# Performance work log

Hardware: AMD Instinct MI355X
Metric: run time of the kernel (lower is better)

## Reference

```python
import jax, jax.numpy as jnp
import numpy as np

QLEN, B, D = 1024, 4, 512
H, DH = 8, 64
MEM, DMLP = 1024, 2048
KLEN = MEM + QLEN
EPS = 1e-5


def layer_norm(x, g, b):
    mu = jnp.mean(x, axis=-1, keepdims=True)
    var = jnp.var(x, axis=-1, keepdims=True)
    return (x - mu) * jax.lax.rsqrt(var + EPS) * g + b


def rel_shift(x):
    # x: [qlen, klen, b, h] -- Transformer-XL relative shift trick
    q, k, b, h = x.shape
    zp = jnp.zeros((q, 1, b, h), dtype=x.dtype)
    x = jnp.concatenate([zp, x], axis=1)          # [q, k+1, b, h]
    x = x.reshape(k + 1, q, b, h)[1:]             # drop first row
    return x.reshape(q, k, b, h)


def setup_inputs() -> dict:
    key = jax.random.key(0)
    ks = jax.random.split(key, 12)
    s = 0.02
    inp = {
        "inputs": jax.random.normal(ks[0], (QLEN, B, D), jnp.float32),
        "r": jax.random.normal(ks[1], (KLEN, D), jnp.float32),
        "u": jax.random.normal(ks[2], (H, DH), jnp.float32) * s,
        "v": jax.random.normal(ks[3], (H, DH), jnp.float32) * s,
        "mem": jax.random.normal(ks[4], (MEM, B, D), jnp.float32),
        # causal mask: query i (global pos MEM+i) cannot attend key j > MEM+i
        "attn_mask": jnp.arange(KLEN)[None, :] > (jnp.arange(QLEN)[:, None] + MEM),
        "Wqkv": jax.random.normal(ks[5], (3 * D, D), jnp.float32) * s,
        "Wr": jax.random.normal(ks[6], (D, D), jnp.float32) * s,
        "Wo": jax.random.normal(ks[7], (D, D), jnp.float32) * s,
        "ln1_g": jnp.ones((D,), jnp.float32),
        "ln1_b": jnp.zeros((D,), jnp.float32),
        "mlp_w1": jax.random.normal(ks[8], (DMLP, D), jnp.float32) * s,
        "mlp_b1": jnp.zeros((DMLP,), jnp.float32),
        "mlp_w2": jax.random.normal(ks[9], (D, DMLP), jnp.float32) * s,
        "mlp_b2": jnp.zeros((D,), jnp.float32),
        "ln2_g": jnp.ones((D,), jnp.float32),
        "ln2_b": jnp.zeros((D,), jnp.float32),
    }
    return inp


def reference(inputs, r, u, v, mem, attn_mask, Wqkv, Wr, Wo,
              ln1_g, ln1_b, mlp_w1, mlp_b1, mlp_w2, mlp_b2, ln2_g, ln2_b):
    qlen, b, d = inputs.shape
    cat = jnp.concatenate([mem, inputs], axis=0)          # [klen, b, d]
    klen = cat.shape[0]
    qkv = cat @ Wqkv.T                                    # [klen, b, 3d]
    q, k, w_v = jnp.split(qkv, 3, axis=-1)
    q = q[-qlen:].reshape(qlen, b, H, DH)
    k = k.reshape(klen, b, H, DH)
    w_v = w_v.reshape(klen, b, H, DH)
    rk = (r @ Wr.T).reshape(klen, H, DH)                  # [klen, h, dh]

    AC = jnp.einsum('ibhd,jbhd->ijbh', q + u, k)          # content term
    BD = jnp.einsum('ibhd,jhd->ijbh', q + v, rk)          # position term
    BD = rel_shift(BD)
    scale = 1.0 / np.sqrt(DH)
    score = (AC + BD) * scale                             # [q, k, b, h]
    score = jnp.where(attn_mask[:, :, None, None], jnp.float32(-1e30), score)
    prob = jax.nn.softmax(score, axis=1)
    attn = jnp.einsum('ijbh,jbhd->ibhd', prob, w_v).reshape(qlen, b, d)
    attn_out = attn @ Wo.T

    y = layer_norm(inputs + attn_out, ln1_g, ln1_b)
    h = jax.nn.relu(y @ mlp_w1.T + mlp_b1)
    z = h @ mlp_w2.T + mlp_b2
    out = layer_norm(y + z, ln2_g, ln2_b)
    return out, prob
```

## Files before the change

### kernel.cpp

```cpp
#include <hip/hip_runtime.h>
#include <math.h>

#define QL 1024
#define BSZ 4
#define DM 512
#define NH 8
#define DHH 64
#define MEML 1024
#define KL 2048
#define DMLP 2048

typedef __attribute__((ext_vector_type(8))) short bf16x8;
typedef __attribute__((ext_vector_type(4))) float f32x4;

#define MFMA16(A, B, C) __builtin_amdgcn_mfma_f32_16x16x32_bf16((A), (B), (C), 0, 0, 0)
#define SWZB(r, cb) (((r) << 7) + ((cb) ^ (((r) & 7) << 4)))
#define RINGB(r, c) (((r) << 9) + ((((c) << 2)) ^ (((r) & 7) << 4)))
#define CVT2(dst, lo, hi) \
  asm("v_cvt_pk_bf16_f32 %0, %1, %2" : "=v"(dst) : "v"(lo), "v"(hi))
#define GLOAD_LDS(gp, lp) __builtin_amdgcn_global_load_lds( \
    (const __attribute__((address_space(1))) void*)(gp), \
    (__attribute__((address_space(3))) void*)(lp), 16, 0, 0)

__device__ __forceinline__ void split_bf16(const float4 a, uint2& h, uint2& l) {
  CVT2(h.x, a.x, a.y); CVT2(h.y, a.z, a.w);
  float4 r;
  r.x = a.x - __uint_as_float(h.x << 16);
  r.y = a.y - __uint_as_float(h.x & 0xffff0000u);
  r.z = a.z - __uint_as_float(h.y << 16);
  r.w = a.w - __uint_as_float(h.y & 0xffff0000u);
  CVT2(l.x, r.x, r.y); CVT2(l.y, r.z, r.w);
}

__device__ __forceinline__ void store_tiled(char* hiB, char* loB, int KT,
                                            int row, int c0, uint2 h, uint2 l) {
  const size_t off = (((size_t)(row >> 7) * KT + (c0 >> 6)) << 14)
                   + SWZB(row & 127, (c0 & 63) * 2);
  *(uint2*)(hiB + off) = h;
  *(uint2*)(loB + off) = l;
}

__global__ __launch_bounds__(256)
void precvt_early(const float* __restrict__ mem, const float* __restrict__ inputs,
                  const float* __restrict__ r, const float* __restrict__ Wqkv,
                  const float* __restrict__ Wr,
                  unsigned short* CAThi, unsigned short* CATlo,
                  unsigned short* Rhi, unsigned short* Rlo,
                  unsigned short* Qhi, unsigned short* Qlo,
                  unsigned short* WrHi, unsigned short* WrLo) {
  const int id = blockIdx.x * 256 + threadIdx.x;
  float4 a; uint2 h, l;
  if (id < 1048576) {
    const int row = id >> 7, c0 = (id & 127) * 4;
    const float* s = (row < 4096) ? mem + (size_t)row * 512
                                  : inputs + (size_t)(row - 4096) * 512;
    a = *(const float4*)(s + c0);
    split_bf16(a, h, l);
    store_tiled((char*)CAThi, (char*)CATlo, 8, row, c0, h, l);
  } else if (id < 1310720) {
    const int e = id - 1048576, row = e >> 7, c0 = (e & 127) * 4;
    a = *(const float4*)(r + (size_t)row * 512 + c0);
    split_bf16(a, h, l);
    store_tiled((char*)Rhi, (char*)Rlo, 8, row, c0, h, l);
  } else if (id < 1507328) {
    const int e = id - 1310720, row = e >> 7, c0 = (e & 127) * 4;
    a = *(const float4*)(Wqkv + (size_t)row * 512 + c0);
    split_bf16(a, h, l);
    store_tiled((char*)Qhi, (char*)Qlo, 8, row, c0, h, l);
  } else if (id < 1572864) {
    const int e = id - 1507328, row = e >> 7, c0 = (e & 127) * 4;
    a = *(const float4*)(Wr + (size_t)row * 512 + c0);
    split_bf16(a, h, l);
    store_tiled((char*)WrHi, (char*)WrLo, 8, row, c0, h, l);
  }
}

__global__ __launch_bounds__(256)
void precvt_late(const float* __restrict__ Wo, const float* __restrict__ w1,
                 const float* __restrict__ w2,
                 unsigned short* WoHi, unsigned short* WoLo,
                 unsigned short* w1Hi, unsigned short* w1Lo,
                 unsigned short* w2Hi, unsigned short* w2Lo) {
  const int id = blockIdx.x * 256 + threadIdx.x;
  float4 a; uint2 h, l;
  if (id < 65536) {
    const int row = id >> 7, c0 = (id & 127) * 4;
    a = *(const float4*)(Wo + (size_t)row * 512 + c0);
    split_bf16(a, h, l);
    store_tiled((char*)WoHi, (char*)WoLo, 8, row, c0, h, l);
  } else if (id < 327680) {
    const int e = id - 65536, row = e >> 7, c0 = (e & 127) * 4;
    a = *(const float4*)(w1 + (size_t)row * 512 + c0);
    split_bf16(a, h, l);
    store_tiled((char*)w1Hi, (char*)w1Lo, 8, row, c0, h, l);
  } else if (id < 589824) {
    const int e = id - 327680, row = e >> 9, c0 = (e & 511) * 4;
    a = *(const float4*)(w2 + (size_t)row * 2048 + c0);
    split_bf16(a, h, l);
    store_tiled((char*)w2Hi, (char*)w2Lo, 32, row, c0, h, l);
  }
}

template<int BM, bool AGLDS, bool BIAS, bool RELU>
__global__ __launch_bounds__(256)
void gemm_nt_mfma(const float* __restrict__ A0, const float* __restrict__ A1, int M0,
                  const unsigned short* __restrict__ AhiT, const unsigned short* __restrict__ AloT,
                  const unsigned short* __restrict__ WhiT, const unsigned short* __restrict__ WloT,
                  const float* __restrict__ bias,
                  float* __restrict__ C, int M, int N, int K) {
  constexpr int MR = 4;
  constexpr int NR = (BM == 128) ? 4 : 2;
  constexpr int AU = BM / 16;
  __shared__ __align__(16) unsigned short Ahi[BM * 64];
  __shared__ __align__(16) unsigned short Alo[BM * 64];
  __shared__ __align__(16) unsigned short Bhi[128 * 64];
  __shared__ __align__(16) unsigned short Blo[128 * 64];

  const int t = threadIdx.x;
  const int w = t >> 6, lane = t & 63;
  const int lq = lane & 15, lg = lane >> 4;
  const int row0 = blockIdx.y * BM, col0 = blockIdx.x * 128;
  const int wrow0 = (BM == 128) ? (w >> 1) * 64 : 0;
  const int wcol0 = (BM == 128) ? (w & 1) * 64 : w * 32;
  const int KT = K >> 6;
  const size_t amt = (size_t)(row0 >> 7) * KT;
  const int asub = (row0 & 127) << 7;
  const size_t bnt = (size_t)(col0 >> 7) * KT;

  float4 paf[AU];
  auto loadA = [&](int k0) {
    if (!AGLDS) {
      #pragma unroll
      for (int it = 0; it < AU; ++it) {
        const int idx = it * 256 + t;
        const int row = idx >> 4, c4 = (idx & 15) * 4;
        const int grow = row0 + row;
        const float* src = (grow < M0) ? (A0 + (size_t)grow * K)
                                       : (A1 + (size_t)(grow - M0) * K);
        paf[it] = *(const float4*)(src + k0 + c4);
      }
    }
  };

  f32x4 acc[MR][NR];
  #pragma unroll
  for (int m = 0; m < MR; ++m)
    #pragma unroll
    for (int n = 0; n < NR; ++n)
      acc[m][n] = (f32x4){0.f, 0.f, 0.f, 0.f};

  loadA(0);
  for (int kt = 0; kt < KT; ++kt) {
    __syncthreads();
    {
      const char* gbh = (const char*)WhiT + ((bnt + kt) << 14);
      const char* gbl = (const char*)WloT + ((bnt + kt) << 14);
      #pragma unroll
      for (int i = 0; i < 4; ++i) {
        const int off = (w * 4 + i) * 1024;
        GLOAD_LDS(gbh + off + lane * 16, (char*)Bhi + off);
        GLOAD_LDS(gbl + off + lane * 16, (char*)Blo + off);
      }
    }
    if (AGLDS) {
      const char* gah = (const char*)AhiT + ((amt + kt) << 14) + asub;
      const char* gal = (const char*)AloT + ((amt + kt) << 14) + asub;
      #pragma unroll
      for (int i = 0; i < BM / 32; ++i) {
        const int off = (w * (BM / 32) + i) * 1024;
        GLOAD_LDS(gah + off + lane * 16, (char*)Ahi + off);
        GLOAD_LDS(gal + off + lane * 16, (char*)Alo + off);
      }
    } else {
      #pragma unroll
      for (int it = 0; it < AU; ++it) {
        const int idx = it * 256 + t;
        const int row = idx >> 4, cb = (idx & 15) * 8;
        uint2 hi, lo;
        split_bf16(paf[it], hi, lo);
        *(uint2*)((char*)Ahi + SWZB(row, cb)) = hi;
        *(uint2*)((char*)Alo + SWZB(row, cb)) = lo;
      }
    }
    __syncthreads();
    if (!AGLDS && kt + 1 < KT) loadA((kt + 1) * 64);
    #pragma unroll
    for (int ks = 0; ks < 2; ++ks) {
      bf16x8 ah[MR], al[MR], bh[NR], bl[NR];
      #pragma unroll
      for (int m = 0; m < MR; ++m) {
        ah[m] = *(const bf16x8*)((const char*)Ahi + SWZB(wrow0 + m * 16 + lq, ks * 64 + lg * 16));
        al[m] = *(const bf16x8*)((const char*)Alo + SWZB(wrow0 + m * 16 + lq, ks * 64 + lg * 16));
      }
      #pragma unroll
      for (int n = 0; n < NR; ++n) {
        bh[n] = *(const bf16x8*)((const char*)Bhi + SWZB(wcol0 + n * 16 + lq, ks * 64 + lg * 16));
        bl[n] = *(const bf16x8*)((const char*)Blo + SWZB(wcol0 + n * 16 + lq, ks * 64 + lg * 16));
      }
      #pragma unroll
      for (int m = 0; m < MR; ++m)
        #pragma unroll
        for (int n = 0; n < NR; ++n) {
          acc[m][n] = MFMA16(ah[m], bh[n], acc[m][n]);
          acc[m][n] = MFMA16(ah[m], bl[n], acc[m][n]);
          acc[m][n] = MFMA16(al[m], bh[n], acc[m][n]);
        }
    }
  }
  #pragma unroll
  for (int n = 0; n < NR; ++n) {
    const int col = col0 + wcol0 + n * 16 + lq;
    const float bv = BIAS ? bias[col] : 0.f;
    #pragma unroll
    for (int m = 0; m < MR; ++m) {
      #pragma unroll
      for (int rg = 0; rg < 4; ++rg) {
        const int row = row0 + wrow0 + m * 16 + lg * 4 + rg;
        float vv = acc[m][n][rg] + bv;
        if (RELU) vv = fmaxf(vv, 0.f);
        C[(size_t)row * N + col] = vv;
      }
    }
  }
}

__global__ __launch_bounds__(256)
void attn2_kernel(const float* __restrict__ QKV, const float* __restrict__ RK,
                  const float* __restrict__ u, const float* __restrict__ v,
                  unsigned short* __restrict__ P, float* __restrict__ INV,
                  float* __restrict__ ATTN) {
  const int b = blockIdx.y;
  const int h = blockIdx.z;
  const int i0 = (((h >> 2) & 1) ? (15 - (int)blockIdx.x) : (int)blockIdx.x) * 64;
  const int t = threadIdx.x;
  const int w = t >> 6;
  const int lane = t & 63;
  const int lq = lane & 15;
  const int lg = lane >> 4;

  __shared__ __align__(16) unsigned short Ks[4096];
  __shared__ __align__(16) unsigned short Rs[4096];
  __shared__ __align__(16) unsigned short Vt[4096];
  __shared__ __align__(16) unsigned short Es[4096];
  __shared__ __align__(16) float Ring[8192];

  {
    const int jr0p = 960 - i0;
    #pragma unroll
    for (int it = 0; it < 4; ++it) {
      const int idx = it * 256 + t;
      const int row = idx >> 4, c4 = (idx & 15) * 4;
      const float4 q4 = *(const float4*)(QKV + ((size_t)(MEML + i0 + row) * 4 + b) * 1536 + h * 64 + c4);
      const float4 u4 = *(const float4*)(u + h * 64 + c4);
      const float4 v4 = *(const float4*)(v + h * 64 + c4);
      uint2 qp;
      CVT2(qp.x, q4.x + u4.x, q4.y + u4.y); CVT2(qp.y, q4.z + u4.z, q4.w + u4.w);
      *(uint2*)((char*)Es + SWZB(row, c4 * 2)) = qp;
      CVT2(qp.x, q4.x + v4.x, q4.y + v4.y); CVT2(qp.y, q4.z + v4.z, q4.w + v4.w);
      *(uint2*)((char*)Ks + SWZB(row, c4 * 2)) = qp;
      const float4 r4 = *(const float4*)(RK + (size_t)(jr0p + row) * 512 + h * 64 + c4);
      CVT2(qp.x, r4.x, r4.y); CVT2(qp.y, r4.z, r4.w);
      *(uint2*)((char*)Rs + SWZB(row, c4 * 2)) = qp;
    }
  }
  __syncthreads();

  float4 pk[4], pr[4], pvv[4];
  auto load_tile = [&](int n) {
    const int j0 = n * 64;
    const int jr0 = j0 - i0 + 1024;
    #pragma unroll
    for (int it = 0; it < 4; ++it) {
      const int idx = it * 256 + t;
      const int row = idx >> 4, c4 = (idx & 15) * 4;
      pk[it] = *(const float4*)(QKV + ((size_t)(j0 + row) * 4 + b) * 1536 + 512 + h * 64 + c4);
      const int jr = jr0 + row;
      float4 r4 = make_float4(0.f, 0.f, 0.f, 0.f);
      if (jr < 2048) r4 = *(const float4*)(RK + (size_t)jr * 512 + h * 64 + c4);
      pr[it] = r4;
    }
    const int jb = (t >> 4) * 4, db = (t & 15) * 4;
    const float* vb = QKV + ((size_t)(j0 + jb) * 4 + b) * 1536 + 1024 + h * 64 + db;
    pvv[0] = *(const float4*)(vb);
    pvv[1] = *(const float4*)(vb + 6144);
    pvv[2] = *(const float4*)(vb + 12288);
    pvv[3] = *(const float4*)(vb + 18432);
  };
  load_tile(0);

  const bf16x8 qu0 = *(const bf16x8*)((const char*)Es + SWZB(w * 16 + lq, lg * 16));
  const bf16x8 qu1 = *(const bf16x8*)((const char*)Es + SWZB(w * 16 + lq, 64 + lg * 16));
  const bf16x8 qv0 = *(const bf16x8*)((const char*)Ks + SWZB(w * 16 + lq, lg * 16));
  const bf16x8 qv1 = *(const bf16x8*)((const char*)Ks + SWZB(w * 16 + lq, 64 + lg * 16));

  {
    f32x4 bd[4];
    #pragma unroll
    for (int nj = 0; nj < 4; ++nj) bd[nj] = (f32x4){0.f, 0.f, 0.f, 0.f};
    #pragma unroll
    for (int nj = 0; nj < 4; ++nj) {
      const bf16x8 rf0 = *(const bf16x8*)((const char*)Rs + SWZB(nj * 16 + lq, lg * 16));
      const bf16x8 rf1 = *(const bf16x8*)((const char*)Rs + SWZB(nj * 16 + lq, 64 + lg * 16));
      bd[nj] = MFMA16(qv0, rf0, bd[nj]);
      bd[nj] = MFMA16(qv1, rf1, bd[nj]);
    }
    #pragma unroll
    for (int nj = 0; nj < 4; ++nj) {
      const int jrl = nj * 16 + lq;
      #pragma unroll
      for (int rg = 0; rg < 4; ++rg) {
        const int il = w * 16 + lg * 4 + rg;
        *(float*)((char*)Ring + RINGB(il, 64 + jrl)) = bd[nj][rg];
      }
    }
  }

  f32x4 pv[4];
  #pragma unroll
  for (int nd = 0; nd < 4; ++nd) pv[nd] = (f32x4){0.f, 0.f, 0.f, 0.f};
  float rs[4] = {0.f, 0.f, 0.f, 0.f};

  const int ntiles = i0 / 64 + 17;
  for (int n = 0; n < ntiles; ++n) {
    const int j0 = n * 64;
    __syncthreads();
    #pragma unroll
    for (int it = 0; it < 4; ++it) {
      const int idx = it * 256 + t;
      const int row = idx >> 4, c4 = (idx & 15) * 4;
      uint2 kp; CVT2(kp.x, pk[it].x, pk[it].y); CVT2(kp.y, pk[it].z, pk[it].w);
      *(uint2*)((char*)Ks + SWZB(row, c4 * 2)) = kp;
      uint2 rp; CVT2(rp.x, pr[it].x, pr[it].y); CVT2(rp.y, pr[it].z, pr[it].w);
      *(uint2*)((char*)Rs + SWZB(row, c4 * 2)) = rp;
    }
    {
      const int jb = (t >> 4) * 4, db = (t & 15) * 4;
      uint2 wv;
      CVT2(wv.x, pvv[0].x, pvv[1].x); CVT2(wv.y, pvv[2].x, pvv[3].x);
      *(uint2*)((char*)Vt + SWZB(db + 0, jb * 2)) = wv;
      CVT2(wv.x, pvv[0].y, pvv[1].y); CVT2(wv.y, pvv[2].y, pvv[3].y);
      *(uint2*)((char*)Vt + SWZB(db + 1, jb * 2)) = wv;
      CVT2(wv.x, pvv[0].z, pvv[1].z); CVT2(wv.y, pvv[2].z, pvv[3].z);
      *(uint2*)((char*)Vt + SWZB(db + 2, jb * 2)) = wv;
      CVT2(wv.x, pvv[0].w, pvv[1].w); CVT2(wv.y, pvv[2].w, pvv[3].w);
      *(uint2*)((char*)Vt + SWZB(db + 3, jb * 2)) = wv;
    }
    __syncthreads();
    if (n + 1 < ntiles) load_tile(n + 1);
    f32x4 acc[4], bdn[4];
    #pragma unroll
    for (int nj = 0; nj < 4; ++nj) {
      acc[nj] = (f32x4){0.f, 0.f, 0.f, 0.f};
      bdn[nj] = (f32x4){0.f, 0.f, 0.f, 0.f};
    }
    #pragma unroll
    for (int nj = 0; nj < 4; ++nj) {
      const bf16x8 kf0 = *(const bf16x8*)((const char*)Ks + SWZB(nj * 16 + lq, lg * 16));
      const bf16x8 rf0 = *(const bf16x8*)((const char*)Rs + SWZB(nj * 16 + lq, lg * 16));
      acc[nj] = MFMA16(qu0, kf0, acc[nj]);
      bdn[nj] = MFMA16(qv0, rf0, bdn[nj]);
      const bf16x8 kf1 = *(const bf16x8*)((const char*)Ks + SWZB(nj * 16 + lq, 64 + lg * 16));
      const bf16x8 rf1 = *(const bf16x8*)((const char*)Rs + SWZB(nj * 16 + lq, 64 + lg * 16));
      acc[nj] = MFMA16(qu1, kf1, acc[nj]);
      bdn[nj] = MFMA16(qv1, rf1, bdn[nj]);
    }
    const int base_cur = (n & 1) * 64;
    const int base_prev = 64 - base_cur;
    #pragma unroll
    for (int nj = 0; nj < 4; ++nj) {
      const int jrl = nj * 16 + lq;
      #pragma unroll
      for (int rg = 0; rg < 4; ++rg) {
        const int il = w * 16 + lg * 4 + rg;
        *(float*)((char*)Ring + RINGB(il, base_cur + jrl)) = bdn[nj][rg];
      }
    }
    #pragma unroll
    for (int njp = 0; njp < 2; ++njp) {
      #pragma unroll
      for (int rg = 0; rg < 4; ++rg) {
        const int il = w * 16 + lg * 4 + rg;
        const int ig = i0 + il;
        float ee[2];
        #pragma unroll
        for (int q2 = 0; q2 < 2; ++q2) {
          const int nj = njp * 2 + q2;
          const int jl = nj * 16 + lq;
          const int jr_rel = jl - il + 63;
          const float ringv = (jr_rel < 64)
              ? *(const float*)((const char*)Ring + RINGB(il, base_prev + jr_rel))
              : *(const float*)((const char*)Ring + RINGB(il, base_cur + jr_rel - 64));
          const float s = 0.125f * (acc[nj][rg] + ringv);
          const float e = (j0 + jl > ig + MEML) ? 0.f : __expf(s);
          rs[rg] += e;
          ee[q2] = e;
        }
        unsigned int pk2; CVT2(pk2, ee[0], ee[1]);
        const int jlA = (njp * 2) * 16 + lq;
        *(unsigned short*)((char*)Es + SWZB(il, jlA * 2)) = (unsigned short)(pk2 & 0xffffu);
        *(unsigned short*)((char*)Es + SWZB(il, (jlA + 16) * 2)) = (unsigned short)(pk2 >> 16);
      }
    }
    {
      const bf16x8 pf0 = *(const bf16x8*)((const char*)Es + SWZB(w * 16 + lq, lg * 16));
      const bf16x8 pf1 = *(const bf16x8*)((const char*)Es + SWZB(w * 16 + lq, 64 + lg * 16));
      #pragma unroll
      for (int nd = 0; nd < 4; ++nd) {
        const bf16x8 vf0 = *(const bf16x8*)((const char*)Vt + SWZB(nd * 16 + lq, lg * 16));
        const bf16x8 vf1 = *(const bf16x8*)((const char*)Vt + SWZB(nd * 16 + lq, 64 + lg * 16));
        pv[nd] = MFMA16(pf0, vf0, pv[nd]);
        pv[nd] = MFMA16(pf1, vf1, pv[nd]);
      }
    }
    #pragma unroll
    for (int it = 0; it < 2; ++it) {
      const int lin = it * 64 + lane;
      const int rr = lin >> 3, c16 = lin & 7;
      const int row = w * 16 + rr;
      const uint4 val = *(const uint4*)((const char*)Es + SWZB(row, c16 * 16));
      *(uint4*)(P + ((size_t)(b * 8 + h) * 1024 + i0 + row) * 2048 + j0 + c16 * 8) = val;
    }
  }

  #pragma unroll
  for (int rg = 0; rg < 4; ++rg) {
    #pragma unroll
    for (int m = 1; m < 16; m <<= 1) rs[rg] += __shfl_xor(rs[rg], m, 64);
  }
  float inv[4];
  #pragma unroll
  for (int rg = 0; rg < 4; ++rg) inv[rg] = 1.0f / rs[rg];
  if (lq == 0) {
    #pragma unroll
    for (int rg = 0; rg < 4; ++rg)
      INV[(size_t)(b * 8 + h) * 1024 + i0 + w * 16 + lg * 4 + rg] = inv[rg];
  }
  #pragma unroll
  for (int nd = 0; nd < 4; ++nd) {
    #pragma unroll
    for (int rg = 0; rg < 4; ++rg) {
      ATTN[((size_t)(i0 + w * 16 + lg * 4 + rg) * 4 + b) * 512 + h * 64 + nd * 16 + lq] =
          pv[nd][rg] * inv[rg];
    }
  }
}

__global__ __launch_bounds__(256)
void ptrans_kernel(const unsigned short* __restrict__ P, const float* __restrict__ INV,
                   float* __restrict__ prob) {
  const int i  = blockIdx.x;
  const int j0 = blockIdx.y * 64;
  const int t  = threadIdx.x;
  __shared__ float tile[32][65];
  __shared__ float invs[32];
  const bool valid = j0 <= (i & ~63) + MEML;
  if (t < 32) invs[t] = INV[(size_t)t * 1024 + i];
  if (valid) {
    const int bh = t >> 3, part = t & 7;
    const uint4 raw = *(const uint4*)(P + ((size_t)bh * 1024 + i) * 2048 + j0 + part * 8);
    const unsigned int w[4] = {raw.x, raw.y, raw.z, raw.w};
    #pragma unroll
    for (int k = 0; k < 4; ++k) {
      tile[bh][part*8 + 2*k]     = __uint_as_float(w[k] << 16);
      tile[bh][part*8 + 2*k + 1] = __uint_as_float(w[k] & 0xffff0000u);
    }
  }
  __syncthreads();
  #pragma unroll
  for (int it = 0; it < 8; ++it) {
    const int idx = it * 256 + t;
    const int jl = idx >> 5, bh = idx & 31;
    const float val = valid ? tile[bh][jl] * invs[bh] : 0.f;
    prob[((size_t)i * 2048 + j0 + jl) * 32 + bh] = val;
  }
}

__global__ __launch_bounds__(256)
void ln_res_kernel(const float* __restrict__ xa, const float* __restrict__ xb,
                   const float* __restrict__ g, const float* __restrict__ bb,
                   float* __restrict__ y) {
  const int rrow = blockIdx.x;
  const int t = threadIdx.x;
  const size_t base = (size_t)rrow * DM;
  __shared__ float red[256];
  const float a0 = xa[base + t]       + xb[base + t];
  const float a1 = xa[base + t + 256] + xb[base + t + 256];
  red[t] = a0 + a1; __syncthreads();
  for (int s = 128; s > 0; s >>= 1) { if (t < s) red[t] += red[t+s]; __syncthreads(); }
  const float mu = red[0] * (1.0f/512.0f);
  __syncthreads();
  red[t] = a0*a0 + a1*a1; __syncthreads();
  for (int s = 128; s > 0; s >>= 1) { if (t < s) red[t] += red[t+s]; __syncthreads(); }
  const float var = red[0] * (1.0f/512.0f) - mu*mu;
  const float w = rsqrtf(var + 1e-5f);
  y[base + t]       = (a0 - mu) * w * g[t]       + bb[t];
  y[base + t + 256] = (a1 - mu) * w * g[t + 256] + bb[t + 256];
}

extern "C" void kernel_launch(void* const* d_in, const int* in_sizes, int n_in,
                              void* d_out, int out_size, void* d_ws, size_t ws_size,
                              hipStream_t stream) {
  const float* inputs = (const float*)d_in[0];
  const float* r      = (const float*)d_in[1];
  const float* u      = (const float*)d_in[2];
  const float* v      = (const float*)d_in[3];
  const float* mem    = (const float*)d_in[4];
  const float* Wqkv   = (const float*)d_in[6];
  const float* Wr     = (const float*)d_in[7];
  const float* Wo     = (const float*)d_in[8];
  const float* ln1g   = (const float*)d_in[9];
  const float* ln1b   = (const float*)d_in[10];
  const float* w1     = (const float*)d_in[11];
  const float* b1     = (const float*)d_in[12];
  const float* w2     = (const float*)d_in[13];
  const float* b2     = (const float*)d_in[14];
  const float* ln2g   = (const float*)d_in[15];
  const float* ln2b   = (const float*)d_in[16];

  float* out  = (float*)d_out;
  float* prob = out + (size_t)QL*BSZ*DM;

  float* ws   = (float*)d_ws;
  unsigned short* P = (unsigned short*)ws;
  float* QKV  = ws + 33554432;
  float* RK   = QKV + 12582912;
  float* ATTN = RK + 1048576;
  float* AO   = ATTN + 2097152;
  float* Y    = AO + 2097152;
  float* INV  = Y + 2097152;
  float* HM   = ws;
  float* Z    = ws + 8388608;

  unsigned short* CAThiT = (unsigned short*)ws;
  unsigned short* CATloT = CAThiT + 4194304;
  unsigned short* RhiT   = CATloT + 4194304;
  unsigned short* RloT   = RhiT + 1048576;
  unsigned short* WqhiT  = RloT + 1048576;
  unsigned short* WqloT  = WqhiT + 786432;
  unsigned short* WrhiT  = WqloT + 786432;
  unsigned short* WrloT  = WrhiT + 262144;
  unsigned short* WohiT = (unsigned short*)(ws + 53510144);
  unsigned short* WoloT = WohiT + 262144;
  unsigned short* w1hiT = WoloT + 262144;
  unsigned short* w1loT = w1hiT + 1048576;
  unsigned short* w2hiT = w1loT + 1048576;
  unsigned short* w2loT = w2hiT + 1048576;

  const dim3 blk256(256);

  precvt_early<<<dim3(6144), blk256, 0, stream>>>(
      mem, inputs, r, Wqkv, Wr,
      CAThiT, CATloT, RhiT, RloT, WqhiT, WqloT, WrhiT, WrloT);
  precvt_late<<<dim3(2304), blk256, 0, stream>>>(
      Wo, w1, w2, WohiT, WoloT, w1hiT, w1loT, w2hiT, w2loT);

  gemm_nt_mfma<128,true,false,false><<<dim3(12, 64), blk256, 0, stream>>>(
      nullptr, nullptr, 0, CAThiT, CATloT, WqhiT, WqloT, nullptr, QKV, 8192, 1536, 512);
  gemm_nt_mfma<64,true,false,false><<<dim3(4, 32), blk256, 0, stream>>>(
      nullptr, nullptr, 0, RhiT, RloT, WrhiT, WrloT, nullptr, RK, 2048, 512, 512);
  attn2_kernel<<<dim3(16, BSZ, NH), blk256, 0, stream>>>(QKV, RK, u, v, P, INV, ATTN);
  ptrans_kernel<<<dim3(1024, 32), blk256, 0, stream>>>(P, INV, prob);

  gemm_nt_mfma<64,false,false,false><<<dim3(4, 64), blk256, 0, stream>>>(
      ATTN, ATTN, 4096, nullptr, nullptr, WohiT, WoloT, nullptr, AO, 4096, 512, 512);
  ln_res_kernel<<<dim3(4096), blk256, 0, stream>>>(inputs, AO, ln1g, ln1b, Y);
  gemm_nt_mfma<128,false,true,true><<<dim3(16, 32), blk256, 0, stream>>>(
      Y, Y, 4096, nullptr, nullptr, w1hiT, w1loT, b1, HM, 4096, 2048, 512);
  gemm_nt_mfma<64,false,true,false><<<dim3(4, 64), blk256, 0, stream>>>(
      HM, HM, 4096, nullptr, nullptr, w2hiT, w2loT, b2, Z, 4096, 512, 2048);
  ln_res_kernel<<<dim3(4096), blk256, 0, stream>>>(Y, Z, ln2g, ln2b, out);
}
```

Baseline: 643.6 us.

## Prepack K/R/V to swizzled bf16 tiles and double-buffer attention loads via LDS DMA

Adds a pack kernel that converts K, RK and transposed V into per-head, pre-swizzled bf16 64-row tiles. The attention kernel then streams K and R tiles straight into double-buffered LDS with global_load_lds, and reads V fragments directly from global memory, which removes the per-tile fp32 loads, conversions and LDS stores from its inner loop. The two weight pre-conversion kernels are merged into a single launch, and the causal mask check is now applied only on the last tile. In exchange there is an extra launch and extra global traffic for the packed copies, the R tile index is clamped at the end of the range, and a pair of LDS tiles is used for the initial BD computation.

After: 660.0 us. 1.03x slower.

```diff
diff --git a/kernel.cpp b/kernel.cpp
--- a/kernel.cpp
+++ b/kernel.cpp
@@ -41,13 +41,17 @@
 }
 
 __global__ __launch_bounds__(256)
-void precvt_early(const float* __restrict__ mem, const float* __restrict__ inputs,
-                  const float* __restrict__ r, const float* __restrict__ Wqkv,
-                  const float* __restrict__ Wr,
-                  unsigned short* CAThi, unsigned short* CATlo,
-                  unsigned short* Rhi, unsigned short* Rlo,
-                  unsigned short* Qhi, unsigned short* Qlo,
-                  unsigned short* WrHi, unsigned short* WrLo) {
+void precvt_all(const float* __restrict__ mem, const float* __restrict__ inputs,
+                const float* __restrict__ r, const float* __restrict__ Wqkv,
+                const float* __restrict__ Wr, const float* __restrict__ Wo,
+                const float* __restrict__ w1, const float* __restrict__ w2,
+                unsigned short* CAThi, unsigned short* CATlo,
+                unsigned short* Rhi, unsigned short* Rlo,
+                unsigned short* Qhi, unsigned short* Qlo,
+                unsigned short* WrHi, unsigned short* WrLo,
+                unsigned short* WoHi, unsigned short* WoLo,
+                unsigned short* w1Hi, unsigned short* w1Lo,
+                unsigned short* w2Hi, unsigned short* w2Lo) {
   const int id = blockIdx.x * 256 + threadIdx.x;
   float4 a; uint2 h, l;
   if (id < 1048576) {
@@ -72,32 +76,67 @@
     a = *(const float4*)(Wr + (size_t)row * 512 + c0);
     split_bf16(a, h, l);
     store_tiled((char*)WrHi, (char*)WrLo, 8, row, c0, h, l);
+  } else if (id < 1638400) {
+    const int e = id - 1572864, row = e >> 7, c0 = (e & 127) * 4;
+    a = *(const float4*)(Wo + (size_t)row * 512 + c0);
+    split_bf16(a, h, l);
+    store_tiled((char*)WoHi, (char*)WoLo, 8, row, c0, h, l);
+  } else if (id < 1900544) {
+    const int e = id - 1638400, row = e >> 7, c0 = (e & 127) * 4;
+    a = *(const float4*)(w1 + (size_t)row * 512 + c0);
+    split_bf16(a, h, l);
+    store_tiled((char*)w1Hi, (char*)w1Lo, 8, row, c0, h, l);
+  } else if (id < 2162688) {
+    const int e = id - 1900544, row = e >> 9, c0 = (e & 511) * 4;
+    a = *(const float4*)(w2 + (size_t)row * 2048 + c0);
+    split_bf16(a, h, l);
+    store_tiled((char*)w2Hi, (char*)w2Lo, 32, row, c0, h, l);
   }
 }
 
 __global__ __launch_bounds__(256)
-void precvt_late(const float* __restrict__ Wo, const float* __restrict__ w1,
-                 const float* __restrict__ w2,
-                 unsigned short* WoHi, unsigned short* WoLo,
-                 unsigned short* w1Hi, unsigned short* w1Lo,
-                 unsigned short* w2Hi, unsigned short* w2Lo) {
+void pack_kvr(const float* __restrict__ QKV, const float* __restrict__ RK,
+              unsigned short* __restrict__ Kb, unsigned short* __restrict__ Rb,
+              unsigned short* __restrict__ Vtb) {
   const int id = blockIdx.x * 256 + threadIdx.x;
-  float4 a; uint2 h, l;
-  if (id < 65536) {
-    const int row = id >> 7, c0 = (id & 127) * 4;
-    a = *(const float4*)(Wo + (size_t)row * 512 + c0);
-    split_bf16(a, h, l);
-    store_tiled((char*)WoHi, (char*)WoLo, 8, row, c0, h, l);
-  } else if (id < 327680) {
-    const int e = id - 65536, row = e >> 7, c0 = (e & 127) * 4;
-    a = *(const float4*)(w1 + (size_t)row * 512 + c0);
-    split_bf16(a, h, l);
-    store_tiled((char*)w1Hi, (char*)w1Lo, 8, row, c0, h, l);
-  } else if (id < 589824) {
-    const int e = id - 327680, row = e >> 9, c0 = (e & 511) * 4;
-    a = *(const float4*)(w2 + (size_t)row * 2048 + c0);
-    split_bf16(a, h, l);
-    store_tiled((char*)w2Hi, (char*)w2Lo, 32, row, c0, h, l);
+  if (id < 1048576) {
+    const int c4 = (id & 15) * 4;
+    const int j  = (id >> 4) & 2047;
+    const int bhv = id >> 15;
+    const int bq = bhv >> 3, hq = bhv & 7;
+    const float4 a = *(const float4*)(QKV + ((size_t)j * 4 + bq) * 1536 + 512 + hq * 64 + c4);
+    uint2 p; CVT2(p.x, a.x, a.y); CVT2(p.y, a.z, a.w);
+    *(uint2*)((char*)Kb + (((size_t)bhv * 32 + (j >> 6)) << 13) + SWZB(j & 63, c4 * 2)) = p;
+  } else if (id < 1310720) {
+    const int e = id - 1048576;
+    const int c4 = (e & 15) * 4;
+    const int jr = (e >> 4) & 2047;
+    const int hq = e >> 15;
+    const float4 a = *(const float4*)(RK + (size_t)jr * 512 + hq * 64 + c4);
+    uint2 p; CVT2(p.x, a.x, a.y); CVT2(p.y, a.z, a.w);
+    *(uint2*)((char*)Rb + (((size_t)hq * 32 + (jr >> 6)) << 13) + SWZB(jr & 63, c4 * 2)) = p;
+  } else if (id < 1572864) {
+    const int e = id - 1310720;
+    const int d4 = (e & 15) * 4;
+    const int jb = ((e >> 4) & 15) * 4;
+    const int jt = (e >> 8) & 31;
+    const int bhv = e >> 13;
+    const int bq = bhv >> 3, hq = bhv & 7;
+    const float* src = QKV + ((size_t)(jt * 64 + jb) * 4 + bq) * 1536 + 1024 + hq * 64 + d4;
+    const float4 a0 = *(const float4*)(src);
+    const float4 a1 = *(const float4*)(src + 6144);
+    const float4 a2 = *(const float4*)(src + 12288);
+    const float4 a3 = *(const float4*)(src + 18432);
+    char* base = (char*)Vtb + (((size_t)bhv * 32 + jt) << 13);
+    uint2 p;
+    CVT2(p.x, a0.x, a1.x); CVT2(p.y, a2.x, a3.x);
+    *(uint2*)(base + (d4 + 0) * 128 + jb * 2) = p;
+    CVT2(p.x, a0.y, a1.y); CVT2(p.y, a2.y, a3.y);
+    *(uint2*)(base + (d4 + 1) * 128 + jb * 2) = p;
+    CVT2(p.x, a0.z, a1.z); CVT2(p.y, a2.z, a3.z);
+    *(uint2*)(base + (d4 + 2) * 128 + jb * 2) = p;
+    CVT2(p.x, a0.w, a1.w); CVT2(p.y, a2.w, a3.w);
+    *(uint2*)(base + (d4 + 3) * 128 + jb * 2) = p;
   }
 }
 
@@ -225,7 +264,10 @@
 }
 
 __global__ __launch_bounds__(256)
-void attn2_kernel(const float* __restrict__ QKV, const float* __restrict__ RK,
+void attn3_kernel(const float* __restrict__ QKV,
+                  const unsigned short* __restrict__ Kb,
+                  const unsigned short* __restrict__ Rb,
+                  const unsigned short* __restrict__ Vtb,
                   const float* __restrict__ u, const float* __restrict__ v,
                   unsigned short* __restrict__ P, float* __restrict__ INV,
                   float* __restrict__ ATTN) {
@@ -237,61 +279,52 @@
   const int lane = t & 63;
   const int lq = lane & 15;
   const int lg = lane >> 4;
-
-  __shared__ __align__(16) unsigned short Ks[4096];
-  __shared__ __align__(16) unsigned short Rs[4096];
-  __shared__ __align__(16) unsigned short Vt[4096];
+  const int bh = b * 8 + h;
+
+  __shared__ __align__(16) unsigned short Ks[2][4096];
+  __shared__ __align__(16) unsigned short Rs[2][4096];
   __shared__ __align__(16) unsigned short Es[4096];
   __shared__ __align__(16) float Ring[8192];
 
+  const int ntiles = i0 / 64 + 17;
+
+  auto dma = [&](int jt, int jrt, int buf) {
+    const char* gk = (const char*)Kb + (((size_t)bh * 32 + jt) << 13);
+    const char* gr = (const char*)Rb + (((size_t)h * 32 + jrt) << 13);
+    const int off = w * 2048;
+    GLOAD_LDS(gk + off + lane * 16, (char*)Ks[buf] + off);
+    GLOAD_LDS(gk + off + 1024 + lane * 16, (char*)Ks[buf] + off + 1024);
+    GLOAD_LDS(gr + off + lane * 16, (char*)Rs[buf] + off);
+    GLOAD_LDS(gr + off + 1024 + lane * 16, (char*)Rs[buf] + off + 1024);
+  };
+
+  dma(0, (1024 - i0) >> 6, 0);
   {
-    const int jr0p = 960 - i0;
-    #pragma unroll
-    for (int it = 0; it < 4; ++it) {
-      const int idx = it * 256 + t;
-      const int row = idx >> 4, c4 = (idx & 15) * 4;
-      const float4 q4 = *(const float4*)(QKV + ((size_t)(MEML + i0 + row) * 4 + b) * 1536 + h * 64 + c4);
-      const float4 u4 = *(const float4*)(u + h * 64 + c4);
-      const float4 v4 = *(const float4*)(v + h * 64 + c4);
-      uint2 qp;
-      CVT2(qp.x, q4.x + u4.x, q4.y + u4.y); CVT2(qp.y, q4.z + u4.z, q4.w + u4.w);
-      *(uint2*)((char*)Es + SWZB(row, c4 * 2)) = qp;
-      CVT2(qp.x, q4.x + v4.x, q4.y + v4.y); CVT2(qp.y, q4.z + v4.z, q4.w + v4.w);
-      *(uint2*)((char*)Ks + SWZB(row, c4 * 2)) = qp;
-      const float4 r4 = *(const float4*)(RK + (size_t)(jr0p + row) * 512 + h * 64 + c4);
-      CVT2(qp.x, r4.x, r4.y); CVT2(qp.y, r4.z, r4.w);
-      *(uint2*)((char*)Rs + SWZB(row, c4 * 2)) = qp;
-    }
+    const int jrtp = (960 - i0) >> 6;
+    const char* gr = (const char*)Rb + (((size_t)h * 32 + jrtp) << 13);
+    const int off = w * 2048;
+    GLOAD_LDS(gr + off + lane * 16, (char*)Rs[1] + off);
+    GLOAD_LDS(gr + off + 1024 + lane * 16, (char*)Rs[1] + off + 1024);
+  }
+  #pragma unroll
+  for (int it = 0; it < 4; ++it) {
+    const int idx = it * 256 + t;
+    const int row = idx >> 4, c4 = (idx & 15) * 4;
+    const float4 q4 = *(const float4*)(QKV + ((size_t)(MEML + i0 + row) * 4 + b) * 1536 + h * 64 + c4);
+    const float4 u4 = *(const float4*)(u + h * 64 + c4);
+    const float4 v4 = *(const float4*)(v + h * 64 + c4);
+    uint2 qp;
+    CVT2(qp.x, q4.x + u4.x, q4.y + u4.y); CVT2(qp.y, q4.z + u4.z, q4.w + u4.w);
+    *(uint2*)((char*)Es + SWZB(row, c4 * 2)) = qp;
+    CVT2(qp.x, q4.x + v4.x, q4.y + v4.y); CVT2(qp.y, q4.z + v4.z, q4.w + v4.w);
+    *(uint2*)((char*)Ks[1] + SWZB(row, c4 * 2)) = qp;
   }
   __syncthreads();
-
-  float4 pk[4], pr[4], pvv[4];
-  auto load_tile = [&](int n) {
-    const int j0 = n * 64;
-    const int jr0 = j0 - i0 + 1024;
-    #pragma unroll
-    for (int it = 0; it < 4; ++it) {
-      const int idx = it * 256 + t;
-      const int row = idx >> 4, c4 = (idx & 15) * 4;
-      pk[it] = *(const float4*)(QKV + ((size_t)(j0 + row) * 4 + b) * 1536 + 512 + h * 64 + c4);
-      const int jr = jr0 + row;
-      float4 r4 = make_float4(0.f, 0.f, 0.f, 0.f);
-      if (jr < 2048) r4 = *(const float4*)(RK + (size_t)jr * 512 + h * 64 + c4);
-      pr[it] = r4;
-    }
-    const int jb = (t >> 4) * 4, db = (t & 15) * 4;
-    const float* vb = QKV + ((size_t)(j0 + jb) * 4 + b) * 1536 + 1024 + h * 64 + db;
-    pvv[0] = *(const float4*)(vb);
-    pvv[1] = *(const float4*)(vb + 6144);
-    pvv[2] = *(const float4*)(vb + 12288);
-    pvv[3] = *(const float4*)(vb + 18432);
-  };
-  load_tile(0);
 
   const bf16x8 qu0 = *(const bf16x8*)((const char*)Es + SWZB(w * 16 + lq, lg * 16));
   const bf16x8 qu1 = *(const bf16x8*)((const char*)Es + SWZB(w * 16 + lq, 64 + lg * 16));
-  const bf16x8 qv0 = *(const bf16x8*)((const char*)Ks + SWZB(w * 16 + lq, lg * 16));
-  const bf16x8 qv1 = *(const bf16x8*)((const char*)Ks + SWZB(w * 16 + lq, 64 + lg * 16));
+  const bf16x8 qv0 = *(const bf16x8*)((const char*)Ks[1] + SWZB(w * 16 + lq, lg * 16));
+  const bf16x8 qv1 = *(const bf16x8*)((const char*)Ks[1] + SWZB(w * 16 + lq, 64 + lg * 16));
 
   {
     f32x4 bd[4];
@@ -299,8 +332,8 @@
     for (int nj = 0; nj < 4; ++nj) bd[nj] = (f32x4){0.f, 0.f, 0.f, 0.f};
     #pragma unroll
     for (int nj = 0; nj < 4; ++nj) {
-      const bf16x8 rf0 = *(const bf16x8*)((const char*)Rs + SWZB(nj * 16 + lq, lg * 16));
-      const bf16x8 rf1 = *(const bf16x8*)((const char*)Rs + SWZB(nj * 16 + lq, 64 + lg * 16));
+      const bf16x8 rf0 = *(const bf16x8*)((const char*)Rs[1] + SWZB(nj * 16 + lq, lg * 16));
+      const bf16x8 rf1 = *(const bf16x8*)((const char*)Rs[1] + SWZB(nj * 16 + lq, 64 + lg * 16));
       bd[nj] = MFMA16(qv0, rf0, bd[nj]);
       bd[nj] = MFMA16(qv1, rf1, bd[nj]);
     }
@@ -320,33 +353,24 @@
   for (int nd = 0; nd < 4; ++nd) pv[nd] = (f32x4){0.f, 0.f, 0.f, 0.f};
   float rs[4] = {0.f, 0.f, 0.f, 0.f};
 
-  const int ntiles = i0 / 64 + 17;
   for (int n = 0; n < ntiles; ++n) {
     const int j0 = n * 64;
+    const int cur = n & 1;
     __syncthreads();
-    #pragma unroll
-    for (int it = 0; it < 4; ++it) {
-      const int idx = it * 256 + t;
-      const int row = idx >> 4, c4 = (idx & 15) * 4;
-      uint2 kp; CVT2(kp.x, pk[it].x, pk[it].y); CVT2(kp.y, pk[it].z, pk[it].w);
-      *(uint2*)((char*)Ks + SWZB(row, c4 * 2)) = kp;
-      uint2 rp; CVT2(rp.x, pr[it].x, pr[it].y); CVT2(rp.y, pr[it].z, pr[it].w);
-      *(uint2*)((char*)Rs + SWZB(row, c4 * 2)) = rp;
-    }
-    {
-      const int jb = (t >> 4) * 4, db = (t & 15) * 4;
-      uint2 wv;
-      CVT2(wv.x, pvv[0].x, pvv[1].x); CVT2(wv.y, pvv[2].x, pvv[3].x);
-      *(uint2*)((char*)Vt + SWZB(db + 0, jb * 2)) = wv;
-      CVT2(wv.x, pvv[0].y, pvv[1].y); CVT2(wv.y, pvv[2].y, pvv[3].y);
-      *(uint2*)((char*)Vt + SWZB(db + 1, jb * 2)) = wv;
-      CVT2(wv.x, pvv[0].z, pvv[1].z); CVT2(wv.y, pvv[2].z, pvv[3].z);
-      *(uint2*)((char*)Vt + SWZB(db + 2, jb * 2)) = wv;
-      CVT2(wv.x, pvv[0].w, pvv[1].w); CVT2(wv.y, pvv[2].w, pvv[3].w);
-      *(uint2*)((char*)Vt + SWZB(db + 3, jb * 2)) = wv;
-    }
-    __syncthreads();
-    if (n + 1 < ntiles) load_tile(n + 1);
+    const char* gv = (const char*)Vtb + (((size_t)bh * 32 + n) << 13);
+    bf16x8 vf0[4], vf1[4];
+    #pragma unroll
+    for (int nd = 0; nd < 4; ++nd) {
+      vf0[nd] = *(const bf16x8*)(gv + (nd * 16 + lq) * 128 + lg * 16);
+      vf1[nd] = *(const bf16x8*)(gv + (nd * 16 + lq) * 128 + 64 + lg * 16);
+    }
+    if (n + 1 < ntiles) {
+      int jrt = ((n + 1) * 64 - i0 + 1024) >> 6;
+      if (jrt > 31) jrt = 31;
+      dma(n + 1, jrt, cur ^ 1);
+    }
+    const char* KsB = (const char*)Ks[cur];
+    const char* RsB = (const char*)Rs[cur];
     f32x4 acc[4], bdn[4];
     #pragma unroll
     for (int nj = 0; nj < 4; ++nj) {
@@ -355,16 +379,16 @@
     }
     #pragma unroll
     for (int nj = 0; nj < 4; ++nj) {
-      const bf16x8 kf0 = *(const bf16x8*)((const char*)Ks + SWZB(nj * 16 + lq, lg * 16));
-      const bf16x8 rf0 = *(const bf16x8*)((const char*)Rs + SWZB(nj * 16 + lq, lg * 16));
+      const bf16x8 kf0 = *(const bf16x8*)(KsB + SWZB(nj * 16 + lq, lg * 16));
+      const bf16x8 rf0 = *(const bf16x8*)(RsB + SWZB(nj * 16 + lq, lg * 16));
       acc[nj] = MFMA16(qu0, kf0, acc[nj]);
       bdn[nj] = MFMA16(qv0, rf0, bdn[nj]);
-      const bf16x8 kf1 = *(const bf16x8*)((const char*)Ks + SWZB(nj * 16 + lq, 64 + lg * 16));
-      const bf16x8 rf1 = *(const bf16x8*)((const char*)Rs + SWZB(nj * 16 + lq, 64 + lg * 16));
+      const bf16x8 kf1 = *(const bf16x8*)(KsB + SWZB(nj * 16 + lq, 64 + lg * 16));
+      const bf16x8 rf1 = *(const bf16x8*)(RsB + SWZB(nj * 16 + lq, 64 + lg * 16));
       acc[nj] = MFMA16(qu1, kf1, acc[nj]);
       bdn[nj] = MFMA16(qv1, rf1, bdn[nj]);
     }
-    const int base_cur = (n & 1) * 64;
+    const int base_cur = cur * 64;
     const int base_prev = 64 - base_cur;
     #pragma unroll
     for (int nj = 0; nj < 4; ++nj) {
@@ -375,12 +399,12 @@
         *(float*)((char*)Ring + RINGB(il, base_cur + jrl)) = bdn[nj][rg];
       }
     }
+    const bool lastm = (n == ntiles - 1);
     #pragma unroll
     for (int njp = 0; njp < 2; ++njp) {
       #pragma unroll
       for (int rg = 0; rg < 4; ++rg) {
         const int il = w * 16 + lg * 4 + rg;
-        const int ig = i0 + il;
         float ee[2];
         #pragma unroll
         for (int q2 = 0; q2 < 2; ++q2) {
@@ -391,7 +415,8 @@
               ? *(const float*)((const char*)Ring + RINGB(il, base_prev + jr_rel))
               : *(const float*)((const char*)Ring + RINGB(il, base_cur + jr_rel - 64));
           const float s = 0.125f * (acc[nj][rg] + ringv);
-          const float e = (j0 + jl > ig + MEML) ? 0.f : __expf(s);
+          float e = __expf(s);
+          if (lastm && jl > il) e = 0.f;
           rs[rg] += e;
           ee[q2] = e;
         }
@@ -406,10 +431,8 @@
       const bf16x8 pf1 = *(const bf16x8*)((const char*)Es + SWZB(w * 16 + lq, 64 + lg * 16));
       #pragma unroll
       for (int nd = 0; nd < 4; ++nd) {
-        const bf16x8 vf0 = *(const bf16x8*)((const char*)Vt + SWZB(nd * 16 + lq, lg * 16));
-        const bf16x8 vf1 = *(const bf16x8*)((const char*)Vt + SWZB(nd * 16 + lq, 64 + lg * 16));
-        pv[nd] = MFMA16(pf0, vf0, pv[nd]);
-        pv[nd] = MFMA16(pf1, vf1, pv[nd]);
+        pv[nd] = MFMA16(pf0, vf0[nd], pv[nd]);
+        pv[nd] = MFMA16(pf1, vf1[nd], pv[nd]);
       }
     }
     #pragma unroll
@@ -418,7 +441,7 @@
       const int rr = lin >> 3, c16 = lin & 7;
       const int row = w * 16 + rr;
       const uint4 val = *(const uint4*)((const char*)Es + SWZB(row, c16 * 16));
-      *(uint4*)(P + ((size_t)(b * 8 + h) * 1024 + i0 + row) * 2048 + j0 + c16 * 8) = val;
+      *(uint4*)(P + ((size_t)bh * 1024 + i0 + row) * 2048 + j0 + c16 * 8) = val;
     }
   }
 
@@ -433,7 +456,7 @@
   if (lq == 0) {
     #pragma unroll
     for (int rg = 0; rg < 4; ++rg)
-      INV[(size_t)(b * 8 + h) * 1024 + i0 + w * 16 + lg * 4 + rg] = inv[rg];
+      INV[(size_t)bh * 1024 + i0 + w * 16 + lg * 4 + rg] = inv[rg];
   }
   #pragma unroll
   for (int nd = 0; nd < 4; ++nd) {
@@ -545,20 +568,24 @@
   unsigned short* w1loT = w1hiT + 1048576;
   unsigned short* w2hiT = w1loT + 1048576;
   unsigned short* w2loT = w2hiT + 1048576;
+  unsigned short* Kb  = (unsigned short*)(ws + 55869440);
+  unsigned short* Vtb = Kb + 4194304;
+  unsigned short* Rb  = Vtb + 4194304;
 
   const dim3 blk256(256);
 
-  precvt_early<<<dim3(6144), blk256, 0, stream>>>(
-      mem, inputs, r, Wqkv, Wr,
-      CAThiT, CATloT, RhiT, RloT, WqhiT, WqloT, WrhiT, WrloT);
-  precvt_late<<<dim3(2304), blk256, 0, stream>>>(
-      Wo, w1, w2, WohiT, WoloT, w1hiT, w1loT, w2hiT, w2loT);
+  precvt_all<<<dim3(8448), blk256, 0, stream>>>(
+      mem, inputs, r, Wqkv, Wr, Wo, w1, w2,
+      CAThiT, CATloT, RhiT, RloT, WqhiT, WqloT, WrhiT, WrloT,
+      WohiT, WoloT, w1hiT, w1loT, w2hiT, w2loT);
 
   gemm_nt_mfma<128,true,false,false><<<dim3(12, 64), blk256, 0, stream>>>(
       nullptr, nullptr, 0, CAThiT, CATloT, WqhiT, WqloT, nullptr, QKV, 8192, 1536, 512);
   gemm_nt_mfma<64,true,false,false><<<dim3(4, 32), blk256, 0, stream>>>(
       nullptr, nullptr, 0, RhiT, RloT, WrhiT, WrloT, nullptr, RK, 2048, 512, 512);
-  attn2_kernel<<<dim3(16, BSZ, NH), blk256, 0, stream>>>(QKV, RK, u, v, P, INV, ATTN);
+  pack_kvr<<<dim3(6144), blk256, 0, stream>>>(QKV, RK, Kb, Rb, Vtb);
+  attn3_kernel<<<dim3(16, BSZ, NH), blk256, 0, stream>>>(
+      QKV, Kb, Rb, Vtb, u, v, P, INV, ATTN);
   ptrans_kernel<<<dim3(1024, 32), blk256, 0, stream>>>(P, INV, prob);
 
   gemm_nt_mfma<64,false,false,false><<<dim3(4, 64), blk256, 0, stream>>>(
```
